# Performance work log

Measured on AMD Instinct MI355X. Metric: run time of the kernel, lower is better.

Reference implementation:

```python
import jax, jax.numpy as jnp
import numpy as np

B, N, D, H, L, M, V, F = 4, 2048, 1024, 16, 4, 256, 32000, 4096
DH = D // H  # 64
KEPS = 1e-4  # performer softmax-kernel eps


def layer_norm(x, g, b, eps=1e-5):
    mu = x.mean(-1, keepdims=True)
    var = ((x - mu) ** 2).mean(-1, keepdims=True)
    return (x - mu) * jax.lax.rsqrt(var + eps) * g + b


def softmax_kernel(data, proj, is_query):
    # data: [B,H,N,DH], proj: [M,DH] -> phi(data): [B,H,N,M]
    dn = data.shape[-1] ** -0.25  # d^{-1/4} normalizer
    ratio = proj.shape[0] ** -0.5
    dd = jnp.einsum('bhnd,md->bhnm', dn * data, proj)
    diag = (data * data).sum(-1, keepdims=True) * 0.5 * dn * dn
    if is_query:
        mx = jnp.max(dd, axis=-1, keepdims=True)
    else:
        mx = jnp.max(dd, axis=(-2, -1), keepdims=True)
    return ratio * (jnp.exp(dd - diag - mx) + KEPS)


def setup_inputs() -> dict:
    key = jax.random.key(0)
    ks = iter(jax.random.split(key, 16))
    p = lambda shape: jax.random.normal(next(ks), shape, jnp.float32) * 0.02
    return {
        'x': jax.random.randint(next(ks), (B, N), 0, V, jnp.int32),
        'mask': jnp.ones((B, N), jnp.bool_),
        'tok_emb': p((V, D)),
        'pos_emb': p((N, D)),
        'ln1_g': jnp.ones((L, D), jnp.float32), 'ln1_b': jnp.zeros((L, D), jnp.float32),
        'wq': p((L, D, D)), 'bq': jnp.zeros((L, D), jnp.float32),
        'wk': p((L, D, D)), 'bk': jnp.zeros((L, D), jnp.float32),
        'wv': p((L, D, D)), 'bv': jnp.zeros((L, D), jnp.float32),
        'wo': p((L, D, D)), 'bo': jnp.zeros((L, D), jnp.float32),
        'proj': jax.random.normal(next(ks), (L, M, DH), jnp.float32),
        'ln2_g': jnp.ones((L, D), jnp.float32), 'ln2_b': jnp.zeros((L, D), jnp.float32),
        'w1': p((L, D, F)), 'b1': jnp.zeros((L, F), jnp.float32),
        'w2': p((L, F, D)), 'b2': jnp.zeros((L, D), jnp.float32),
    }


def reference(x, mask, tok_emb, pos_emb, ln1_g, ln1_b, wq, bq, wk, bk, wv, bv,
              wo, bo, proj, ln2_g, ln2_b, w1, b1, w2, b2):
    h = tok_emb[x] + pos_emb[jnp.arange(N)]  # [B,N,D]
    mask4 = mask[:, None, :, None]  # [B,1,N,1]

    def split_heads(t):  # [B,N,D] -> [B,H,N,DH]
        return t.reshape(B, N, H, DH).transpose(0, 2, 1, 3)

    def layer(h, params):
        (g1, c1, Wq, Bq, Wk, Bk, Wv, Bv, Wo, Bo, P, g2, c2, W1, B1, W2, B2) = params
        z = layer_norm(h, g1, c1)
        q = split_heads(z @ Wq + Bq)
        k = split_heads(z @ Wk + Bk)
        v = split_heads(z @ Wv + Bv)
        v = jnp.where(mask4, v, 0.0)  # performer masks only v
        qp = softmax_kernel(q, P, True)   # [B,H,N,M]
        kp = softmax_kernel(k, P, False)  # [B,H,N,M]
        d_inv = 1.0 / jnp.einsum('bhnm,bhm->bhn', qp, kp.sum(-2))
        ctx = jnp.einsum('bhnm,bhnd->bhmd', kp, v)  # [B,H,M,DH]
        attn = jnp.einsum('bhmd,bhnm,bhn->bhnd', ctx, qp, d_inv)
        attn = attn.transpose(0, 2, 1, 3).reshape(B, N, D)
        h = h + attn @ Wo + Bo
        z = layer_norm(h, g2, c2)
        h = h + jax.nn.gelu(z @ W1 + B1, approximate=False) @ W2 + B2
        return h, None

    h, _ = jax.lax.scan(layer, h, (ln1_g, ln1_b, wq, bq, wk, bk, wv, bv,
                                   wo, bo, proj, ln2_g, ln2_b, w1, b1, w2, b2))
    return h.mean(1)  # [B,D]
```

## Files before the change

kernel.cpp:

```cpp
#include <hip/hip_runtime.h>
#include <hip/hip_bf16.h>

typedef unsigned short u16;
typedef unsigned int u32;
typedef __attribute__((ext_vector_type(8))) short short8v;
typedef __attribute__((ext_vector_type(4))) float f32x4;

#define BB    4
#define NN    2048
#define DDIM  1024
#define HH    16
#define DH    64
#define MM    256
#define FDIM  4096
#define LL    4
#define QLD   3072

static constexpr float DN_    = 0.35355339059327373f;
static constexpr float RATIO_ = 0.0625f;
static constexpr float KEPS_  = 1e-4f;

__device__ __forceinline__ short f2bs(float f) {
  __hip_bfloat16 h = __float2bfloat16(f);
  return *(short*)&h;
}
__device__ __forceinline__ float bs2f(short s) {
  return __uint_as_float(((unsigned)(u16)s) << 16);
}

__device__ __forceinline__ void gload_lds16(const void* g, void* l) {
  __builtin_amdgcn_global_load_lds(
      (const __attribute__((address_space(1))) u32*)g,
      (__attribute__((address_space(3))) u32*)l, 16, 0, 0);
}

__global__ __launch_bounds__(256) void k_sentinel(float* __restrict__ out, float val) {
  int i = blockIdx.x * 256 + threadIdx.x;
  if (i < BB * DDIM) out[i] = val;
}

__global__ __launch_bounds__(256) void k_embed(const int* __restrict__ x,
    const float* __restrict__ tok, const float* __restrict__ pos,
    float* __restrict__ h) {
  int r = blockIdx.x;
  int n = r & (NN - 1);
  int id = x[r];
  const float* tr = tok + (size_t)id * DDIM;
  const float* pr = pos + (size_t)n * DDIM;
  float* hr = h + (size_t)r * DDIM;
  for (int d = threadIdx.x; d < DDIM; d += 256)
    hr[d] = tr[d] + pr[d];
}

__global__ __launch_bounds__(256) void k_ln(const float* __restrict__ in,
    const float* __restrict__ g, const float* __restrict__ b,
    __hip_bfloat16* __restrict__ out) {
  int r = blockIdx.x, t = threadIdx.x;
  const float* xr = in + (size_t)r * DDIM;
  float v[4], s = 0.f, s2 = 0.f;
#pragma unroll
  for (int i = 0; i < 4; i++) {
    v[i] = xr[t + i * 256];
    s += v[i]; s2 += v[i] * v[i];
  }
#pragma unroll
  for (int o = 32; o > 0; o >>= 1) { s += __shfl_down(s, o); s2 += __shfl_down(s2, o); }
  __shared__ float ws[8];
  int wid = t >> 6, lane = t & 63;
  if (lane == 0) { ws[wid] = s; ws[4 + wid] = s2; }
  __syncthreads();
  s = ws[0] + ws[1] + ws[2] + ws[3];
  s2 = ws[4] + ws[5] + ws[6] + ws[7];
  float mu = s * (1.f / DDIM);
  float var = s2 * (1.f / DDIM) - mu * mu;
  float rstd = rsqrtf(var + 1e-5f);
  __hip_bfloat16* orow = out + (size_t)r * DDIM;
#pragma unroll
  for (int i = 0; i < 4; i++) {
    int d = t + i * 256;
    orow[d] = __float2bfloat16((v[i] - mu) * rstd * g[d] + b[d]);
  }
}

__global__ __launch_bounds__(256) void k_wt(const float* __restrict__ W,
    __hip_bfloat16* __restrict__ Wt, int K, int N) {
  __shared__ float tl[64][68];
  int t = threadIdx.x;
  int n0 = blockIdx.x * 64, k0 = blockIdx.y * 64;
#pragma unroll
  for (int i = 0; i < 4; i++) {
    int kl = (t >> 4) + i * 16;
    float4 f = *(const float4*)&W[(size_t)(k0 + kl) * N + n0 + (t & 15) * 4];
    tl[kl][(t & 15) * 4 + 0] = f.x;
    tl[kl][(t & 15) * 4 + 1] = f.y;
    tl[kl][(t & 15) * 4 + 2] = f.z;
    tl[kl][(t & 15) * 4 + 3] = f.w;
  }
  __syncthreads();
  int nl = t >> 2;
#pragma unroll
  for (int i = 0; i < 4; i++) {
    int kl = (t & 3) * 4 + i * 16;
    size_t ob = (size_t)(n0 + nl) * K + k0 + kl;
    Wt[ob + 0] = __float2bfloat16(tl[kl + 0][nl]);
    Wt[ob + 1] = __float2bfloat16(tl[kl + 1][nl]);
    Wt[ob + 2] = __float2bfloat16(tl[kl + 2][nl]);
    Wt[ob + 3] = __float2bfloat16(tl[kl + 3][nl]);
  }
}

__global__ __launch_bounds__(256) void k_catb(const float* __restrict__ bq,
    const float* __restrict__ bk, const float* __restrict__ bv,
    float* __restrict__ dst) {
  int i = blockIdx.x * 256 + threadIdx.x;
  dst[i] = i < 1024 ? bq[i] : (i < 2048 ? bk[i - 1024] : bv[i - 2048]);
}

template <bool GELU, bool RES, bool OUTF32>
__global__ __launch_bounds__(256) void k_gemm_mfma(
    const u16* __restrict__ A, const u16* __restrict__ Bt,
    const float* __restrict__ bias, const float* __restrict__ Cin,
    void* __restrict__ Cout, int M, int K, int Nc) {
  __shared__ short As[2][128 * 32];
  __shared__ short Bs[2][128 * 32];
  int t = threadIdx.x;
  int lane = t & 63, w = t >> 6;
  int wr = w >> 1, wc = w & 1;
  int nwg = gridDim.x * gridDim.y;
  int id = blockIdx.y * gridDim.x + blockIdx.x;
  int swz = (id & 7) * (nwg >> 3) + (id >> 3);
  int bx = swz % gridDim.x, by = swz / gridDim.x;
  int row0 = by * 128, col0 = bx * 128;
  f32x4 acc[4][4];
  f32x4 z4 = {0.f, 0.f, 0.f, 0.f};
#pragma unroll
  for (int i = 0; i < 4; i++)
#pragma unroll
    for (int j = 0; j < 4; j++) acc[i][j] = z4;
  int fr = lane & 15;
  int fc = lane >> 4;
  int c0 = t, c1 = 256 + t;
  int r0 = c0 >> 2, cl0 = (c0 & 3) ^ ((r0 >> 1) & 3);
  int r1 = c1 >> 2, cl1 = (c1 & 3) ^ ((r1 >> 1) & 3);
  const u16* Arow0 = A + (size_t)(row0 + r0) * K + cl0 * 8;
  const u16* Arow1 = A + (size_t)(row0 + r1) * K + cl1 * 8;
  const u16* Brow0 = Bt + (size_t)(col0 + r0) * K + cl0 * 8;
  const u16* Brow1 = Bt + (size_t)(col0 + r1) * K + cl1 * 8;

  auto STG = [&](int bi, int kk) {
    gload_lds16(Arow0 + kk, As[bi] + c0 * 8);
    gload_lds16(Arow1 + kk, As[bi] + c1 * 8);
    gload_lds16(Brow0 + kk, Bs[bi] + c0 * 8);
    gload_lds16(Brow1 + kk, Bs[bi] + c1 * 8);
  };
  auto COMPUTE = [&](int bi) {
    short8v af[4], bfr[4];
#pragma unroll
    for (int f = 0; f < 4; f++) {
      int ra = wr * 64 + f * 16 + fr;
      af[f] = *(const short8v*)(As[bi] + ra * 32 + (fc ^ ((ra >> 1) & 3)) * 8);
      int rb = wc * 64 + f * 16 + fr;
      bfr[f] = *(const short8v*)(Bs[bi] + rb * 32 + (fc ^ ((rb >> 1) & 3)) * 8);
    }
#pragma unroll
    for (int fi = 0; fi < 4; fi++)
#pragma unroll
      for (int fj = 0; fj < 4; fj++)
        acc[fi][fj] = __builtin_amdgcn_mfma_f32_16x16x32_bf16(
            af[fi], bfr[fj], acc[fi][fj], 0, 0, 0);
  };

  STG(0, 0);
  __syncthreads();
  int cur = 0;
  for (int k0 = 0; k0 + 32 < K; k0 += 32) {
    STG(cur ^ 1, k0 + 32);
    COMPUTE(cur);
    __syncthreads();
    cur ^= 1;
  }
  COMPUTE(cur);
#pragma unroll
  for (int fi = 0; fi < 4; fi++) {
#pragma unroll
    for (int fj = 0; fj < 4; fj++) {
#pragma unroll
      for (int ri = 0; ri < 4; ri++) {
        int row = row0 + wr * 64 + fi * 16 + (lane >> 4) * 4 + ri;
        int col = col0 + wc * 64 + fj * 16 + fr;
        float vv = acc[fi][fj][ri] + bias[col];
        if (GELU) vv = 0.5f * vv * (1.f + erff(vv * 0.70710678118f));
        if (RES) vv += Cin[(size_t)row * Nc + col];
        if (OUTF32) ((float*)Cout)[(size_t)row * Nc + col] = vv;
        else ((__hip_bfloat16*)Cout)[(size_t)row * Nc + col] = __float2bfloat16(vv);
      }
    }
  }
}

__global__ __launch_bounds__(256) void k_kv(const u16* __restrict__ kq,
    const u16* __restrict__ vq, const float* __restrict__ P,
    float* __restrict__ es, float* __restrict__ mxc, float* __restrict__ svc,
    float* __restrict__ ctx_part) {
  int bh = blockIdx.x >> 2, chunk = blockIdx.x & 3;
  int b = bh >> 4, hh = bh & 15;
  int t = threadIdx.x, lane = t & 63, w = t >> 6;
  int fr = lane & 15, kc = lane >> 4;
  __shared__ short Pl[256 * 64];
  __shared__ short ksl[32 * 64];
  __shared__ short vtl[64 * 32];
  __shared__ short kpl[256 * 32];
  __shared__ float dgs[32];
  __shared__ float wredk[4];
  __shared__ float svl[32][64];
#pragma unroll
  for (int i = 0; i < 8; i++) {
    int e = i * 256 + t;
    int m = e >> 3, j = e & 7;
    float4 f0 = *(const float4*)&P[m * 64 + j * 8];
    float4 f1 = *(const float4*)&P[m * 64 + j * 8 + 4];
    short* dst = Pl + m * 64 + ((j ^ (m & 7)) << 3);
    dst[0] = f2bs(f0.x); dst[1] = f2bs(f0.y); dst[2] = f2bs(f0.z); dst[3] = f2bs(f0.w);
    dst[4] = f2bs(f1.x); dst[5] = f2bs(f1.y); dst[6] = f2bs(f1.z); dst[7] = f2bs(f1.w);
  }
  f32x4 z4 = {0.f, 0.f, 0.f, 0.f};
  f32x4 accc[4][4];
#pragma unroll
  for (int i = 0; i < 4; i++)
#pragma unroll
    for (int j = 0; j < 4; j++) accc[i][j] = z4;
  float ksp[4] = {0.f, 0.f, 0.f, 0.f};
  float svp[8] = {0.f, 0.f, 0.f, 0.f, 0.f, 0.f, 0.f, 0.f};
  float m_run = -3e38f;
  int r8 = t >> 3, j8 = t & 7;
  for (int tile = 0; tile < 16; ++tile) {
    int n0 = chunk * 512 + tile * 32;
    __syncthreads();
    {
      size_t gk = ((size_t)(b * NN) + n0 + r8) * QLD + hh * 64 + j8 * 8;
      short8v k8 = *(const short8v*)(kq + gk);
      *(short8v*)(ksl + r8 * 64 + ((j8 ^ (r8 & 7)) << 3)) = k8;
      float s2 = 0.f;
#pragma unroll
      for (int ii = 0; ii < 8; ii++) { float rv = bs2f(k8[ii]); s2 += rv * rv; }
      s2 += __shfl_down(s2, 4); s2 += __shfl_down(s2, 2); s2 += __shfl_down(s2, 1);
      if (j8 == 0) dgs[r8] = 0.0625f * s2;
      short8v v8 = *(const short8v*)(vq + gk);
#pragma unroll
      for (int ii = 0; ii < 8; ii++) {
        int d = j8 * 8 + ii;
        vtl[d * 32 + (((r8 >> 3) ^ ((d >> 1) & 3)) << 3) + (r8 & 7)] = v8[ii];
        svp[ii] += bs2f(v8[ii]);
      }
    }
    __syncthreads();
    f32x4 accd[2][4];
#pragma unroll
    for (int nt = 0; nt < 2; nt++)
#pragma unroll
      for (int mt = 0; mt < 4; mt++) accd[nt][mt] = z4;
#pragma unroll
    for (int s = 0; s < 2; s++) {
      short8v afr[2];
#pragma unroll
      for (int nt = 0; nt < 2; nt++) {
        int rr = nt * 16 + fr;
        afr[nt] = *(const short8v*)(ksl + rr * 64 + (((s * 4 + kc) ^ (rr & 7)) << 3));
      }
#pragma unroll
      for (int mt = 0; mt < 4; mt++) {
        int m = w * 64 + mt * 16 + fr;
        short8v bfp = *(const short8v*)(Pl + m * 64 + (((s * 4 + kc) ^ (m & 7)) << 3));
#pragma unroll
        for (int nt = 0; nt < 2; nt++)
          accd[nt][mt] = __builtin_amdgcn_mfma_f32_16x16x32_bf16(afr[nt], bfp, accd[nt][mt], 0, 0, 0);
      }
    }
    float tm = -3e38f;
#pragma unroll
    for (int nt = 0; nt < 2; nt++)
#pragma unroll
      for (int mt = 0; mt < 4; mt++) {
        accd[nt][mt] = accd[nt][mt] * DN_;
        tm = fmaxf(tm, fmaxf(fmaxf(accd[nt][mt][0], accd[nt][mt][1]),
                             fmaxf(accd[nt][mt][2], accd[nt][mt][3])));
      }
#pragma unroll
    for (int o = 32; o > 0; o >>= 1) tm = fmaxf(tm, __shfl_xor(tm, o));
    if (lane == 0) wredk[w] = tm;
    __syncthreads();
    float bm = fmaxf(fmaxf(wredk[0], wredk[1]), fmaxf(wredk[2], wredk[3]));
    float nm = fmaxf(m_run, bm);
    float fac = expf(m_run - nm);
#pragma unroll
    for (int mt = 0; mt < 4; mt++) {
      ksp[mt] *= fac;
#pragma unroll
      for (int dt = 0; dt < 4; dt++) accc[mt][dt] = accc[mt][dt] * fac;
    }
    m_run = nm;
#pragma unroll
    for (int nt = 0; nt < 2; nt++)
#pragma unroll
      for (int mt = 0; mt < 4; mt++)
#pragma unroll
        for (int ri = 0; ri < 4; ri++) {
          int n = nt * 16 + kc * 4 + ri;
          int m = w * 64 + mt * 16 + fr;
          float kpv = expf(accd[nt][mt][ri] - dgs[n] - m_run);
          ksp[mt] += kpv;
          kpl[m * 32 + (((n >> 3) ^ ((m >> 1) & 3)) << 3) + (n & 7)] = f2bs(kpv);
        }
    short8v bvv[4];
#pragma unroll
    for (int dt = 0; dt < 4; dt++) {
      int d = dt * 16 + fr;
      bvv[dt] = *(const short8v*)(vtl + d * 32 + ((kc ^ ((d >> 1) & 3)) << 3));
    }
#pragma unroll
    for (int mt = 0; mt < 4; mt++) {
      int m = w * 64 + mt * 16 + fr;
      short8v ak = *(const short8v*)(kpl + m * 32 + ((kc ^ ((m >> 1) & 3)) << 3));
#pragma unroll
      for (int dt = 0; dt < 4; dt++)
        accc[mt][dt] = __builtin_amdgcn_mfma_f32_16x16x32_bf16(ak, bvv[dt], accc[mt][dt], 0, 0, 0);
    }
  }
#pragma unroll
  for (int mt = 0; mt < 4; mt++) {
    float vv = ksp[mt];
    vv += __shfl_xor(vv, 16);
    vv += __shfl_xor(vv, 32);
    if (lane < 16)
      es[((size_t)bh * 4 + chunk) * MM + w * 64 + mt * 16 + lane] = vv;
  }
  if (t == 0) mxc[bh * 4 + chunk] = m_run;
#pragma unroll
  for (int ii = 0; ii < 8; ii++) svl[r8][j8 * 8 + ii] = svp[ii];
  __syncthreads();
  if (t < 64) {
    float s = 0.f;
#pragma unroll
    for (int r = 0; r < 32; r++) s += svl[r][t];
    svc[((size_t)bh * 4 + chunk) * 64 + t] = s;
  }
  size_t base = ((size_t)(chunk * 64 + bh)) * MM * DH;
#pragma unroll
  for (int mt = 0; mt < 4; mt++)
#pragma unroll
    for (int dt = 0; dt < 4; dt++)
#pragma unroll
      for (int ri = 0; ri < 4; ri++) {
        int m = w * 64 + mt * 16 + kc * 4 + ri;
        int d = dt * 16 + fr;
        ctx_part[base + m * 64 + d] = accc[mt][dt][ri];
      }
}

__global__ __launch_bounds__(256) void k_ctxred(const float* __restrict__ part,
    const float* __restrict__ es, const float* __restrict__ mxc,
    const float* __restrict__ svc, float* __restrict__ ksum,
    u16* __restrict__ ctxT) {
  int bh = blockIdx.x, t = threadIdx.x;
  __shared__ float tl[64][65];
  __shared__ float facs[4];
  __shared__ float svg[64];
  float mg = fmaxf(fmaxf(mxc[bh * 4 + 0], mxc[bh * 4 + 1]),
                   fmaxf(mxc[bh * 4 + 2], mxc[bh * 4 + 3]));
  if (t < 4) facs[t] = expf(mxc[bh * 4 + t] - mg);
  if (t >= 64 && t < 128) {
    int d = t - 64;
    svg[d] = svc[((size_t)bh * 4 + 0) * 64 + d] + svc[((size_t)bh * 4 + 1) * 64 + d] +
             svc[((size_t)bh * 4 + 2) * 64 + d] + svc[((size_t)bh * 4 + 3) * 64 + d];
  }
  __syncthreads();
  float f0 = facs[0], f1 = facs[1], f2 = facs[2], f3 = facs[3];
  {
    size_t eb = (size_t)bh * 4 * MM;
    float s = es[eb + t] * f0 + es[eb + MM + t] * f1 +
              es[eb + 2 * MM + t] * f2 + es[eb + 3 * MM + t] * f3;
    ksum[bh * MM + t] = RATIO_ * (s + KEPS_ * 2048.0f);
  }
  const size_t CH = (size_t)64 * MM * DH;
  for (int mt = 0; mt < 4; mt++) {
    __syncthreads();
#pragma unroll
    for (int i = 0; i < 16; i++) {
      int e = i * 256 + t;
      int ml = e >> 6, d = e & 63;
      size_t off = (size_t)bh * MM * DH + (size_t)(mt * 64 + ml) * 64 + d;
      float ev = part[off] * f0 + part[CH + off] * f1 +
                 part[2 * CH + off] * f2 + part[3 * CH + off] * f3;
      tl[ml][d] = RATIO_ * (ev + KEPS_ * svg[d]);
    }
    __syncthreads();
#pragma unroll
    for (int i = 0; i < 16; i++) {
      int e = i * 256 + t;
      int d = e >> 6, ml = e & 63;
      ctxT[((size_t)bh * 64 + d) * 256 + mt * 64 + ml] = (u16)f2bs(tl[ml][d]);
    }
  }
}

__global__ __launch_bounds__(256) void k_attn_fused(const u16* __restrict__ q,
    const float* __restrict__ P, const float* __restrict__ ksum,
    const u16* __restrict__ ctxT, __hip_bfloat16* __restrict__ attn) {
  int bh = blockIdx.x >> 5, rb = blockIdx.x & 31;
  int b = bh >> 4, hh = bh & 15;
  int n0 = rb * 64;
  int t = threadIdx.x, lane = t & 63, w = t >> 6;
  int fr = lane & 15, kc = lane >> 4;
  __shared__ short qsl[64 * 64];
  __shared__ short qpl[64 * 256];
  __shared__ short ctl[64 * 256];
  __shared__ float dgs[64];
  __shared__ float ks_l[MM];
  __shared__ float wred[4][64];
  __shared__ float mx_l[64];
  __shared__ float inv_l[64];
  short8v pf[4][2];
#pragma unroll
  for (int mt = 0; mt < 4; mt++)
#pragma unroll
    for (int s = 0; s < 2; s++) {
      int m = w * 64 + mt * 16 + fr;
      const float* src = P + m * 64 + s * 32 + kc * 8;
      float4 f0 = *(const float4*)src;
      float4 f1 = *(const float4*)(src + 4);
      short8v pv;
      pv[0] = f2bs(f0.x); pv[1] = f2bs(f0.y); pv[2] = f2bs(f0.z); pv[3] = f2bs(f0.w);
      pv[4] = f2bs(f1.x); pv[5] = f2bs(f1.y); pv[6] = f2bs(f1.z); pv[7] = f2bs(f1.w);
      pf[mt][s] = pv;
    }
  ks_l[t] = ksum[bh * MM + t];
  {
    int rr = t >> 2, j4 = t & 3;
    size_t gq = ((size_t)(b * NN) + n0 + rr) * QLD + hh * 64 + j4 * 16;
    short8v q0 = *(const short8v*)(q + gq);
    short8v q1 = *(const short8v*)(q + gq + 8);
    *(short8v*)(qsl + rr * 64 + (((2 * j4) ^ (rr & 7)) << 3)) = q0;
    *(short8v*)(qsl + rr * 64 + (((2 * j4 + 1) ^ (rr & 7)) << 3)) = q1;
    float s2 = 0.f;
#pragma unroll
    for (int ii = 0; ii < 8; ii++) {
      float a = bs2f(q0[ii]), c = bs2f(q1[ii]);
      s2 += a * a + c * c;
    }
    s2 += __shfl_down(s2, 2); s2 += __shfl_down(s2, 1);
    if (j4 == 0) dgs[rr] = 0.0625f * s2;
  }
#pragma unroll
  for (int i = 0; i < 8; i++) {
    int e = i * 256 + t;
    int d = e >> 5, c = e & 31;
    short8v cv = *(const short8v*)(ctxT + ((size_t)bh * 64 + d) * 256 + c * 8);
    *(short8v*)(ctl + d * 256 + ((c ^ (d & 7)) << 3)) = cv;
  }
  __syncthreads();
  f32x4 z4 = {0.f, 0.f, 0.f, 0.f};
  f32x4 accd[4][4];
#pragma unroll
  for (int i = 0; i < 4; i++)
#pragma unroll
    for (int j = 0; j < 4; j++) accd[i][j] = z4;
#pragma unroll
  for (int s = 0; s < 2; s++) {
    short8v afr[4];
#pragma unroll
    for (int nt = 0; nt < 4; nt++) {
      int rr = nt * 16 + fr;
      afr[nt] = *(const short8v*)(qsl + rr * 64 + (((s * 4 + kc) ^ (rr & 7)) << 3));
    }
#pragma unroll
    for (int mt = 0; mt < 4; mt++)
#pragma unroll
      for (int nt = 0; nt < 4; nt++)
        accd[nt][mt] = __builtin_amdgcn_mfma_f32_16x16x32_bf16(afr[nt], pf[mt][s], accd[nt][mt], 0, 0, 0);
  }
#pragma unroll
  for (int i = 0; i < 4; i++)
#pragma unroll
    for (int j = 0; j < 4; j++) accd[i][j] = accd[i][j] * DN_;
  {
    float pmx[16];
#pragma unroll
    for (int nt = 0; nt < 4; nt++)
#pragma unroll
      for (int ri = 0; ri < 4; ri++) {
        float m_ = fmaxf(fmaxf(accd[nt][0][ri], accd[nt][1][ri]),
                         fmaxf(accd[nt][2][ri], accd[nt][3][ri]));
#pragma unroll
        for (int o = 1; o < 16; o <<= 1) m_ = fmaxf(m_, __shfl_xor(m_, o));
        pmx[nt * 4 + ri] = m_;
      }
    if (fr == 0) {
#pragma unroll
      for (int nt = 0; nt < 4; nt++)
#pragma unroll
        for (int ri = 0; ri < 4; ri++)
          wred[w][nt * 16 + kc * 4 + ri] = pmx[nt * 4 + ri];
    }
  }
  __syncthreads();
  if (t < 64)
    mx_l[t] = fmaxf(fmaxf(wred[0][t], wred[1][t]), fmaxf(wred[2][t], wred[3][t]));
  __syncthreads();
  {
    float sp[16];
#pragma unroll
    for (int i = 0; i < 16; i++) sp[i] = 0.f;
#pragma unroll
    for (int nt = 0; nt < 4; nt++)
#pragma unroll
      for (int mt = 0; mt < 4; mt++)
#pragma unroll
        for (int ri = 0; ri < 4; ri++) {
          int n = nt * 16 + kc * 4 + ri;
          int m = w * 64 + mt * 16 + fr;
          float kpv = RATIO_ * (expf(accd[nt][mt][ri] - dgs[n] - mx_l[n]) + KEPS_);
          sp[nt * 4 + ri] += kpv * ks_l[m];
          int c = m >> 3;
          qpl[n * 256 + ((c ^ (n & 7)) << 3) + (m & 7)] = f2bs(kpv);
        }
#pragma unroll
    for (int i = 0; i < 16; i++) {
#pragma unroll
      for (int o = 1; o < 16; o <<= 1) sp[i] += __shfl_xor(sp[i], o);
    }
    if (fr == 0) {
#pragma unroll
      for (int nt = 0; nt < 4; nt++)
#pragma unroll
        for (int ri = 0; ri < 4; ri++)
          wred[w][nt * 16 + kc * 4 + ri] = sp[nt * 4 + ri];
    }
  }
  __syncthreads();
  if (t < 64)
    inv_l[t] = 1.f / (wred[0][t] + wred[1][t] + wred[2][t] + wred[3][t]);
  __syncthreads();
  f32x4 acc2[4];
#pragma unroll
  for (int dt = 0; dt < 4; dt++) acc2[dt] = z4;
  int nrow = w * 16 + fr;
#pragma unroll
  for (int ks = 0; ks < 8; ks++) {
    int c = ks * 4 + kc;
    short8v aq = *(const short8v*)(qpl + nrow * 256 + ((c ^ (nrow & 7)) << 3));
#pragma unroll
    for (int dt = 0; dt < 4; dt++) {
      int d = dt * 16 + fr;
      short8v bc = *(const short8v*)(ctl + d * 256 + ((c ^ (d & 7)) << 3));
      acc2[dt] = __builtin_amdgcn_mfma_f32_16x16x32_bf16(aq, bc, acc2[dt], 0, 0, 0);
    }
  }
#pragma unroll
  for (int dt = 0; dt < 4; dt++)
#pragma unroll
    for (int ri = 0; ri < 4; ri++) {
      int n = w * 16 + kc * 4 + ri;
      int d = dt * 16 + fr;
      attn[((size_t)(b * NN) + n0 + n) * DDIM + hh * 64 + d] =
          __float2bfloat16(acc2[dt][ri] * inv_l[n]);
    }
}

__global__ __launch_bounds__(256) void k_mean1(const float* __restrict__ h,
                                               float* __restrict__ part) {
  int c = blockIdx.x >> 2, b = blockIdx.x & 3;
  int t = threadIdx.x;
  float s0 = 0.f, s1 = 0.f, s2 = 0.f, s3 = 0.f;
  for (int n = c * 32; n < c * 32 + 32; n++) {
    float4 f = *(const float4*)&h[((size_t)b * NN + n) * DDIM + t * 4];
    s0 += f.x; s1 += f.y; s2 += f.z; s3 += f.w;
  }
  float* p = part + (size_t)c * (BB * DDIM) + b * DDIM + t * 4;
  p[0] = s0; p[1] = s1; p[2] = s2; p[3] = s3;
}
__global__ __launch_bounds__(256) void k_mean2(const float* __restrict__ part,
                                               float* __restrict__ out) {
  int idx = blockIdx.x * 256 + threadIdx.x;
  float s = 0.f;
  for (int c = 0; c < 64; c++) s += part[(size_t)c * (BB * DDIM) + idx];
  out[idx] = s * (1.f / NN);
}

extern "C" void kernel_launch(void* const* d_in, const int* in_sizes, int n_in,
                              void* d_out, int out_size, void* d_ws, size_t ws_size,
                              hipStream_t stream) {
  static const long long EXP[21] = {
      8192, 8192, 32768000, 2097152, 4096, 4096,
      4194304, 4096, 4194304, 4096, 4194304, 4096, 4194304, 4096,
      65536, 4096, 4096, 16777216, 16384, 16777216, 4096
  };
  const size_t NEED_WS = 197559552;
  float sentinel = 0.f;
  if (n_in != 21) {
    sentinel = 100000.f + 100.f * (float)n_in;
  } else {
    for (int i = 0; i < 21; i++)
      if ((long long)in_sizes[i] != EXP[i]) { sentinel = 1000.f + 100.f * i; break; }
  }
  if (sentinel == 0.f && out_size != BB * DDIM) sentinel = 6000.f;
  if (sentinel == 0.f && ws_size < NEED_WS) {
    float units = (float)(ws_size / (32ull << 20));
    if (units > 40.f) units = 40.f;
    sentinel = 5000.f + 100.f * units;
  }
  if (sentinel != 0.f) {
    k_sentinel<<<16, 256, 0, stream>>>((float*)d_out, sentinel);
    return;
  }

  const int* x = (const int*)d_in[0];
  const float* tok  = (const float*)d_in[2];
  const float* pos  = (const float*)d_in[3];
  const float* ln1g = (const float*)d_in[4];
  const float* ln1b = (const float*)d_in[5];
  const float* wq   = (const float*)d_in[6];
  const float* bq   = (const float*)d_in[7];
  const float* wk   = (const float*)d_in[8];
  const float* bk   = (const float*)d_in[9];
  const float* wv   = (const float*)d_in[10];
  const float* bv   = (const float*)d_in[11];
  const float* wo   = (const float*)d_in[12];
  const float* bo   = (const float*)d_in[13];
  const float* proj = (const float*)d_in[14];
  const float* ln2g = (const float*)d_in[15];
  const float* ln2b = (const float*)d_in[16];
  const float* w1   = (const float*)d_in[17];
  const float* b1   = (const float*)d_in[18];
  const float* w2   = (const float*)d_in[19];
  const float* b2   = (const float*)d_in[20];

  const int BN = BB * NN;
  const size_t SZ = (size_t)BN * DDIM;
  const size_t MEG = 1048576;
  float* ws    = (float*)d_ws;
  float* h     = ws;
  u16* qkvb    = (u16*)(ws + SZ);
  __hip_bfloat16* zb   = (__hip_bfloat16*)(ws + 4 * SZ);
  float* ctx   = ws + 4 * SZ + SZ / 2;
  float* ksum  = ctx + (size_t)BB * HH * MM * DH;
  float* bmaxp = ksum + BB * HH * MM;
  float* bcat  = bmaxp + 4096;
  float* mxp   = bmaxp + BB * HH * 128;
  __hip_bfloat16* wt = (__hip_bfloat16*)(mxp + 64);
  float* ctxp  = (float*)(wt + 12 * MEG);
  float* esb   = ctxp + 4 * MEG;
  float* mxcb  = esb + 65536;
  float* svcb  = mxcb + 256;
  u16* ctxT    = (u16*)ctx;
  __hip_bfloat16* ff1b = (__hip_bfloat16*)qkvb;
  __hip_bfloat16* zab  = (__hip_bfloat16*)ctxp;
  float* meanp = ctxp;

  k_embed<<<BN, 256, 0, stream>>>(x, tok, pos, h);

  for (int l = 0; l < LL; l++) {
    const float* Wq = wq + (size_t)l * DDIM * DDIM;
    const float* Wk = wk + (size_t)l * DDIM * DDIM;
    const float* Wv = wv + (size_t)l * DDIM * DDIM;
    const float* Wo = wo + (size_t)l * DDIM * DDIM;
    const float* W1 = w1 + (size_t)l * DDIM * FDIM;
    const float* W2 = w2 + (size_t)l * FDIM * DDIM;
    const float* Pl = proj + (size_t)l * MM * DH;
    __hip_bfloat16* wtq = wt;
    __hip_bfloat16* wtk = wt + 1 * MEG;
    __hip_bfloat16* wtv = wt + 2 * MEG;
    __hip_bfloat16* wto = wt + 3 * MEG;
    __hip_bfloat16* wt1 = wt + 4 * MEG;
    __hip_bfloat16* wt2 = wt + 8 * MEG;

    k_wt<<<dim3(16, 16), 256, 0, stream>>>(Wq, wtq, DDIM, DDIM);
    k_wt<<<dim3(16, 16), 256, 0, stream>>>(Wk, wtk, DDIM, DDIM);
    k_wt<<<dim3(16, 16), 256, 0, stream>>>(Wv, wtv, DDIM, DDIM);
    k_wt<<<dim3(16, 16), 256, 0, stream>>>(Wo, wto, DDIM, DDIM);
    k_wt<<<dim3(64, 16), 256, 0, stream>>>(W1, wt1, DDIM, FDIM);
    k_wt<<<dim3(16, 64), 256, 0, stream>>>(W2, wt2, FDIM, DDIM);
    k_catb<<<12, 256, 0, stream>>>(bq + l * DDIM, bk + l * DDIM, bv + l * DDIM, bcat);

    k_ln<<<BN, 256, 0, stream>>>(h, ln1g + l * DDIM, ln1b + l * DDIM, zb);

    dim3 gQKV(QLD / 128, BN / 128);
    k_gemm_mfma<false, false, false><<<gQKV, 256, 0, stream>>>(
        (const u16*)zb, (const u16*)wtq, bcat, nullptr, qkvb, BN, DDIM, QLD);

    k_kv<<<BB * HH * 4, 256, 0, stream>>>(qkvb + 1024, qkvb + 2048, Pl,
                                          esb, mxcb, svcb, ctxp);
    k_ctxred<<<BB * HH, 256, 0, stream>>>(ctxp, esb, mxcb, svcb, ksum, ctxT);
    k_attn_fused<<<BB * HH * 32, 256, 0, stream>>>(qkvb, Pl, ksum, ctxT, zab);

    dim3 gO(DDIM / 128, BN / 128);
    k_gemm_mfma<false, true, true><<<gO, 256, 0, stream>>>(
        (const u16*)zab, (const u16*)wto, bo + l * DDIM, h, h, BN, DDIM, DDIM);

    k_ln<<<BN, 256, 0, stream>>>(h, ln2g + l * DDIM, ln2b + l * DDIM, zb);
    dim3 g1(FDIM / 128, BN / 128);
    k_gemm_mfma<true, false, false><<<g1, 256, 0, stream>>>(
        (const u16*)zb, (const u16*)wt1, b1 + l * FDIM, nullptr, ff1b, BN, DDIM, FDIM);
    dim3 g2(DDIM / 128, BN / 128);
    k_gemm_mfma<false, true, true><<<g2, 256, 0, stream>>>(
        (const u16*)ff1b, (const u16*)wt2, b2 + l * DDIM, h, h, BN, FDIM, DDIM);
  }

  k_mean1<<<256, 256, 0, stream>>>(h, meanp);
  k_mean2<<<16, 256, 0, stream>>>(meanp, (float*)d_out);
}
```

Before: 2.079 ms.

## Fuse embed with LN, batch weight transposes, split k_kv over feature halves

Several unrelated changes land together. Embedding is fused with the first LayerNorm. The six per-layer weight-transpose launches and the bias concat are merged into one kernel. k_kv is split across two halves of the random-feature dimension, doubling its grid, and each half keeps its own running max, which k_ctxred reconciles. erff in the GELU epilogue is replaced by a polynomial erf approximation, and expf by __expf. The goals are fewer launches, better CU occupancy for the key/value reduction and cheaper transcendentals, at the cost of small numerical deviations.

```diff
diff --git a/kernel.cpp b/kernel.cpp
--- a/kernel.cpp
+++ b/kernel.cpp
@@ -27,6 +27,14 @@
 __device__ __forceinline__ float bs2f(short s) {
   return __uint_as_float(((unsigned)(u16)s) << 16);
 }
+__device__ __forceinline__ float erf_fast(float x) {
+  float ax = fabsf(x);
+  float t = 1.f / (1.f + 0.3275911f * ax);
+  float y = t * (0.254829592f + t * (-0.284496736f + t * (1.421413741f +
+            t * (-1.453152027f + t * 1.061405429f))));
+  float r = 1.f - y * __expf(-ax * ax);
+  return copysignf(r, x);
+}
 
 __device__ __forceinline__ void gload_lds16(const void* g, void* l) {
   __builtin_amdgcn_global_load_lds(
@@ -39,17 +47,41 @@
   if (i < BB * DDIM) out[i] = val;
 }
 
-__global__ __launch_bounds__(256) void k_embed(const int* __restrict__ x,
+__global__ __launch_bounds__(256) void k_embed_ln(const int* __restrict__ x,
     const float* __restrict__ tok, const float* __restrict__ pos,
-    float* __restrict__ h) {
-  int r = blockIdx.x;
+    const float* __restrict__ g, const float* __restrict__ b,
+    float* __restrict__ h, __hip_bfloat16* __restrict__ zb) {
+  int r = blockIdx.x, t = threadIdx.x;
   int n = r & (NN - 1);
   int id = x[r];
   const float* tr = tok + (size_t)id * DDIM;
   const float* pr = pos + (size_t)n * DDIM;
   float* hr = h + (size_t)r * DDIM;
-  for (int d = threadIdx.x; d < DDIM; d += 256)
-    hr[d] = tr[d] + pr[d];
+  float v[4], s = 0.f, s2 = 0.f;
+#pragma unroll
+  for (int i = 0; i < 4; i++) {
+    int d = t + i * 256;
+    v[i] = tr[d] + pr[d];
+    hr[d] = v[i];
+    s += v[i]; s2 += v[i] * v[i];
+  }
+#pragma unroll
+  for (int o = 32; o > 0; o >>= 1) { s += __shfl_down(s, o); s2 += __shfl_down(s2, o); }
+  __shared__ float ws[8];
+  int wid = t >> 6, lane = t & 63;
+  if (lane == 0) { ws[wid] = s; ws[4 + wid] = s2; }
+  __syncthreads();
+  s = ws[0] + ws[1] + ws[2] + ws[3];
+  s2 = ws[4] + ws[5] + ws[6] + ws[7];
+  float mu = s * (1.f / DDIM);
+  float var = s2 * (1.f / DDIM) - mu * mu;
+  float rstd = rsqrtf(var + 1e-5f);
+  __hip_bfloat16* orow = zb + (size_t)r * DDIM;
+#pragma unroll
+  for (int i = 0; i < 4; i++) {
+    int d = t + i * 256;
+    orow[d] = __float2bfloat16((v[i] - mu) * rstd * g[d] + b[d]);
+  }
 }
 
 __global__ __launch_bounds__(256) void k_ln(const float* __restrict__ in,
@@ -82,11 +114,40 @@
   }
 }
 
-__global__ __launch_bounds__(256) void k_wt(const float* __restrict__ W,
-    __hip_bfloat16* __restrict__ Wt, int K, int N) {
+__global__ __launch_bounds__(256) void k_wtall(const float* __restrict__ Wq,
+    const float* __restrict__ Wk, const float* __restrict__ Wv,
+    const float* __restrict__ Wo, const float* __restrict__ W1,
+    const float* __restrict__ W2, const float* __restrict__ bq,
+    const float* __restrict__ bk, const float* __restrict__ bv,
+    __hip_bfloat16* __restrict__ wt, float* __restrict__ bcat) {
+  int id = blockIdx.x;
+  int t = threadIdx.x;
+  if (id >= 3072) {
+    int i = (id - 3072) * 256 + t;
+    bcat[i] = i < 1024 ? bq[i] : (i < 2048 ? bk[i - 1024] : bv[i - 2048]);
+    return;
+  }
+  const float* W;
+  __hip_bfloat16* Wt;
+  int K, N, n0, k0;
+  if (id < 1024) {
+    int which = id >> 8, local = id & 255;
+    W = which == 0 ? Wq : which == 1 ? Wk : which == 2 ? Wv : Wo;
+    Wt = wt + (size_t)which * 1048576;
+    K = 1024; N = 1024;
+    n0 = (local & 15) * 64; k0 = (local >> 4) * 64;
+  } else if (id < 2048) {
+    int local = id - 1024;
+    W = W1; Wt = wt + (size_t)4 * 1048576;
+    K = 1024; N = 4096;
+    n0 = (local & 63) * 64; k0 = (local >> 6) * 64;
+  } else {
+    int local = id - 2048;
+    W = W2; Wt = wt + (size_t)8 * 1048576;
+    K = 4096; N = 1024;
+    n0 = (local & 15) * 64; k0 = (local >> 4) * 64;
+  }
   __shared__ float tl[64][68];
-  int t = threadIdx.x;
-  int n0 = blockIdx.x * 64, k0 = blockIdx.y * 64;
 #pragma unroll
   for (int i = 0; i < 4; i++) {
     int kl = (t >> 4) + i * 16;
@@ -107,13 +168,6 @@
     Wt[ob + 2] = __float2bfloat16(tl[kl + 2][nl]);
     Wt[ob + 3] = __float2bfloat16(tl[kl + 3][nl]);
   }
-}
-
-__global__ __launch_bounds__(256) void k_catb(const float* __restrict__ bq,
-    const float* __restrict__ bk, const float* __restrict__ bv,
-    float* __restrict__ dst) {
-  int i = blockIdx.x * 256 + threadIdx.x;
-  dst[i] = i < 1024 ? bq[i] : (i < 2048 ? bk[i - 1024] : bv[i - 2048]);
 }
 
 template <bool GELU, bool RES, bool OUTF32>
@@ -189,7 +243,7 @@
         int row = row0 + wr * 64 + fi * 16 + (lane >> 4) * 4 + ri;
         int col = col0 + wc * 64 + fj * 16 + fr;
         float vv = acc[fi][fj][ri] + bias[col];
-        if (GELU) vv = 0.5f * vv * (1.f + erff(vv * 0.70710678118f));
+        if (GELU) vv = 0.5f * vv * (1.f + erf_fast(vv * 0.70710678118f));
         if (RES) vv += Cin[(size_t)row * Nc + col];
         if (OUTF32) ((float*)Cout)[(size_t)row * Nc + col] = vv;
         else ((__hip_bfloat16*)Cout)[(size_t)row * Nc + col] = __float2bfloat16(vv);
@@ -202,34 +256,37 @@
     const u16* __restrict__ vq, const float* __restrict__ P,
     float* __restrict__ es, float* __restrict__ mxc, float* __restrict__ svc,
     float* __restrict__ ctx_part) {
-  int bh = blockIdx.x >> 2, chunk = blockIdx.x & 3;
+  int bh = blockIdx.x >> 3;
+  int chunk = (blockIdx.x >> 1) & 3;
+  int mh = blockIdx.x & 1;
   int b = bh >> 4, hh = bh & 15;
   int t = threadIdx.x, lane = t & 63, w = t >> 6;
   int fr = lane & 15, kc = lane >> 4;
-  __shared__ short Pl[256 * 64];
+  __shared__ short Pl[128 * 64];
   __shared__ short ksl[32 * 64];
   __shared__ short vtl[64 * 32];
-  __shared__ short kpl[256 * 32];
+  __shared__ short kpl[128 * 32];
   __shared__ float dgs[32];
   __shared__ float wredk[4];
   __shared__ float svl[32][64];
 #pragma unroll
-  for (int i = 0; i < 8; i++) {
+  for (int i = 0; i < 4; i++) {
     int e = i * 256 + t;
     int m = e >> 3, j = e & 7;
-    float4 f0 = *(const float4*)&P[m * 64 + j * 8];
-    float4 f1 = *(const float4*)&P[m * 64 + j * 8 + 4];
+    const float* src = P + (size_t)(mh * 128 + m) * 64 + j * 8;
+    float4 f0 = *(const float4*)src;
+    float4 f1 = *(const float4*)(src + 4);
     short* dst = Pl + m * 64 + ((j ^ (m & 7)) << 3);
     dst[0] = f2bs(f0.x); dst[1] = f2bs(f0.y); dst[2] = f2bs(f0.z); dst[3] = f2bs(f0.w);
     dst[4] = f2bs(f1.x); dst[5] = f2bs(f1.y); dst[6] = f2bs(f1.z); dst[7] = f2bs(f1.w);
   }
   f32x4 z4 = {0.f, 0.f, 0.f, 0.f};
-  f32x4 accc[4][4];
-#pragma unroll
-  for (int i = 0; i < 4; i++)
+  f32x4 accc[2][4];
+#pragma unroll
+  for (int i = 0; i < 2; i++)
 #pragma unroll
     for (int j = 0; j < 4; j++) accc[i][j] = z4;
-  float ksp[4] = {0.f, 0.f, 0.f, 0.f};
+  float ksp[2] = {0.f, 0.f};
   float svp[8] = {0.f, 0.f, 0.f, 0.f, 0.f, 0.f, 0.f, 0.f};
   float m_run = -3e38f;
   int r8 = t >> 3, j8 = t & 7;
@@ -254,11 +311,11 @@
       }
     }
     __syncthreads();
-    f32x4 accd[2][4];
+    f32x4 accd[2][2];
 #pragma unroll
     for (int nt = 0; nt < 2; nt++)
 #pragma unroll
-      for (int mt = 0; mt < 4; mt++) accd[nt][mt] = z4;
+      for (int mt = 0; mt < 2; mt++) accd[nt][mt] = z4;
 #pragma unroll
     for (int s = 0; s < 2; s++) {
       short8v afr[2];
@@ -268,9 +325,9 @@
         afr[nt] = *(const short8v*)(ksl + rr * 64 + (((s * 4 + kc) ^ (rr & 7)) << 3));
       }
 #pragma unroll
-      for (int mt = 0; mt < 4; mt++) {
-        int m = w * 64 + mt * 16 + fr;
-        short8v bfp = *(const short8v*)(Pl + m * 64 + (((s * 4 + kc) ^ (m & 7)) << 3));
+      for (int mt = 0; mt < 2; mt++) {
+        int ml = w * 32 + mt * 16 + fr;
+        short8v bfp = *(const short8v*)(Pl + ml * 64 + (((s * 4 + kc) ^ (ml & 7)) << 3));
 #pragma unroll
         for (int nt = 0; nt < 2; nt++)
           accd[nt][mt] = __builtin_amdgcn_mfma_f32_16x16x32_bf16(afr[nt], bfp, accd[nt][mt], 0, 0, 0);
@@ -280,7 +337,7 @@
 #pragma unroll
     for (int nt = 0; nt < 2; nt++)
 #pragma unroll
-      for (int mt = 0; mt < 4; mt++) {
+      for (int mt = 0; mt < 2; mt++) {
         accd[nt][mt] = accd[nt][mt] * DN_;
         tm = fmaxf(tm, fmaxf(fmaxf(accd[nt][mt][0], accd[nt][mt][1]),
                              fmaxf(accd[nt][mt][2], accd[nt][mt][3])));
@@ -291,9 +348,9 @@
     __syncthreads();
     float bm = fmaxf(fmaxf(wredk[0], wredk[1]), fmaxf(wredk[2], wredk[3]));
     float nm = fmaxf(m_run, bm);
-    float fac = expf(m_run - nm);
-#pragma unroll
-    for (int mt = 0; mt < 4; mt++) {
+    float fac = __expf(m_run - nm);
+#pragma unroll
+    for (int mt = 0; mt < 2; mt++) {
       ksp[mt] *= fac;
 #pragma unroll
       for (int dt = 0; dt < 4; dt++) accc[mt][dt] = accc[mt][dt] * fac;
@@ -302,14 +359,14 @@
 #pragma unroll
     for (int nt = 0; nt < 2; nt++)
 #pragma unroll
-      for (int mt = 0; mt < 4; mt++)
+      for (int mt = 0; mt < 2; mt++)
 #pragma unroll
         for (int ri = 0; ri < 4; ri++) {
           int n = nt * 16 + kc * 4 + ri;
-          int m = w * 64 + mt * 16 + fr;
-          float kpv = expf(accd[nt][mt][ri] - dgs[n] - m_run);
+          int ml = w * 32 + mt * 16 + fr;
+          float kpv = __expf(accd[nt][mt][ri] - dgs[n] - m_run);
           ksp[mt] += kpv;
-          kpl[m * 32 + (((n >> 3) ^ ((m >> 1) & 3)) << 3) + (n & 7)] = f2bs(kpv);
+          kpl[ml * 32 + (((n >> 3) ^ ((ml >> 1) & 3)) << 3) + (n & 7)] = f2bs(kpv);
         }
     short8v bvv[4];
 #pragma unroll
@@ -318,27 +375,27 @@
       bvv[dt] = *(const short8v*)(vtl + d * 32 + ((kc ^ ((d >> 1) & 3)) << 3));
     }
 #pragma unroll
-    for (int mt = 0; mt < 4; mt++) {
-      int m = w * 64 + mt * 16 + fr;
-      short8v ak = *(const short8v*)(kpl + m * 32 + ((kc ^ ((m >> 1) & 3)) << 3));
+    for (int mt = 0; mt < 2; mt++) {
+      int ml = w * 32 + mt * 16 + fr;
+      short8v ak = *(const short8v*)(kpl + ml * 32 + ((kc ^ ((ml >> 1) & 3)) << 3));
 #pragma unroll
       for (int dt = 0; dt < 4; dt++)
         accc[mt][dt] = __builtin_amdgcn_mfma_f32_16x16x32_bf16(ak, bvv[dt], accc[mt][dt], 0, 0, 0);
     }
   }
 #pragma unroll
-  for (int mt = 0; mt < 4; mt++) {
+  for (int mt = 0; mt < 2; mt++) {
     float vv = ksp[mt];
     vv += __shfl_xor(vv, 16);
     vv += __shfl_xor(vv, 32);
     if (lane < 16)
-      es[((size_t)bh * 4 + chunk) * MM + w * 64 + mt * 16 + lane] = vv;
-  }
-  if (t == 0) mxc[bh * 4 + chunk] = m_run;
+      es[((size_t)bh * 4 + chunk) * MM + mh * 128 + w * 32 + mt * 16 + lane] = vv;
+  }
+  if (t == 0) mxc[((size_t)bh * 4 + chunk) * 2 + mh] = m_run;
 #pragma unroll
   for (int ii = 0; ii < 8; ii++) svl[r8][j8 * 8 + ii] = svp[ii];
   __syncthreads();
-  if (t < 64) {
+  if (mh == 0 && t < 64) {
     float s = 0.f;
 #pragma unroll
     for (int r = 0; r < 32; r++) s += svl[r][t];
@@ -346,14 +403,14 @@
   }
   size_t base = ((size_t)(chunk * 64 + bh)) * MM * DH;
 #pragma unroll
-  for (int mt = 0; mt < 4; mt++)
+  for (int mt = 0; mt < 2; mt++)
 #pragma unroll
     for (int dt = 0; dt < 4; dt++)
 #pragma unroll
       for (int ri = 0; ri < 4; ri++) {
-        int m = w * 64 + mt * 16 + kc * 4 + ri;
+        int mg = mh * 128 + w * 32 + mt * 16 + kc * 4 + ri;
         int d = dt * 16 + fr;
-        ctx_part[base + m * 64 + d] = accc[mt][dt][ri];
+        ctx_part[base + mg * 64 + d] = accc[mt][dt][ri];
       }
 }
 
@@ -363,26 +420,30 @@
     u16* __restrict__ ctxT) {
   int bh = blockIdx.x, t = threadIdx.x;
   __shared__ float tl[64][65];
-  __shared__ float facs[4];
+  __shared__ float facs[8];
   __shared__ float svg[64];
-  float mg = fmaxf(fmaxf(mxc[bh * 4 + 0], mxc[bh * 4 + 1]),
-                   fmaxf(mxc[bh * 4 + 2], mxc[bh * 4 + 3]));
-  if (t < 4) facs[t] = expf(mxc[bh * 4 + t] - mg);
+  float mg = -3e38f;
+#pragma unroll
+  for (int i = 0; i < 8; i++) mg = fmaxf(mg, mxc[(size_t)bh * 8 + i]);
+  if (t < 8) facs[t] = __expf(mxc[(size_t)bh * 8 + t] - mg);
   if (t >= 64 && t < 128) {
     int d = t - 64;
     svg[d] = svc[((size_t)bh * 4 + 0) * 64 + d] + svc[((size_t)bh * 4 + 1) * 64 + d] +
              svc[((size_t)bh * 4 + 2) * 64 + d] + svc[((size_t)bh * 4 + 3) * 64 + d];
   }
   __syncthreads();
-  float f0 = facs[0], f1 = facs[1], f2 = facs[2], f3 = facs[3];
   {
     size_t eb = (size_t)bh * 4 * MM;
-    float s = es[eb + t] * f0 + es[eb + MM + t] * f1 +
-              es[eb + 2 * MM + t] * f2 + es[eb + 3 * MM + t] * f3;
+    int mhb = t >> 7;
+    float s = es[eb + t] * facs[0 * 2 + mhb] + es[eb + MM + t] * facs[1 * 2 + mhb] +
+              es[eb + 2 * MM + t] * facs[2 * 2 + mhb] + es[eb + 3 * MM + t] * facs[3 * 2 + mhb];
     ksum[bh * MM + t] = RATIO_ * (s + KEPS_ * 2048.0f);
   }
   const size_t CH = (size_t)64 * MM * DH;
   for (int mt = 0; mt < 4; mt++) {
+    int mhb = mt >> 1;
+    float f0 = facs[0 * 2 + mhb], f1 = facs[1 * 2 + mhb];
+    float f2 = facs[2 * 2 + mhb], f3 = facs[3 * 2 + mhb];
     __syncthreads();
 #pragma unroll
     for (int i = 0; i < 16; i++) {
@@ -518,7 +579,7 @@
         for (int ri = 0; ri < 4; ri++) {
           int n = nt * 16 + kc * 4 + ri;
           int m = w * 64 + mt * 16 + fr;
-          float kpv = RATIO_ * (expf(accd[nt][mt][ri] - dgs[n] - mx_l[n]) + KEPS_);
+          float kpv = RATIO_ * (__expf(accd[nt][mt][ri] - dgs[n] - mx_l[n]) + KEPS_);
           sp[nt * 4 + ri] += kpv * ks_l[m];
           int c = m >> 3;
           qpl[n * 256 + ((c ^ (n & 7)) << 3) + (m & 7)] = f2bs(kpv);
@@ -650,13 +711,13 @@
   float* ctxp  = (float*)(wt + 12 * MEG);
   float* esb   = ctxp + 4 * MEG;
   float* mxcb  = esb + 65536;
-  float* svcb  = mxcb + 256;
+  float* svcb  = mxcb + 512;
   u16* ctxT    = (u16*)ctx;
   __hip_bfloat16* ff1b = (__hip_bfloat16*)qkvb;
   __hip_bfloat16* zab  = (__hip_bfloat16*)ctxp;
   float* meanp = ctxp;
 
-  k_embed<<<BN, 256, 0, stream>>>(x, tok, pos, h);
+  k_embed_ln<<<BN, 256, 0, stream>>>(x, tok, pos, ln1g, ln1b, h, zb);
 
   for (int l = 0; l < LL; l++) {
     const float* Wq = wq + (size_t)l * DDIM * DDIM;
@@ -667,27 +728,22 @@
     const float* W2 = w2 + (size_t)l * FDIM * DDIM;
     const float* Pl = proj + (size_t)l * MM * DH;
     __hip_bfloat16* wtq = wt;
-    __hip_bfloat16* wtk = wt + 1 * MEG;
-    __hip_bfloat16* wtv = wt + 2 * MEG;
     __hip_bfloat16* wto = wt + 3 * MEG;
     __hip_bfloat16* wt1 = wt + 4 * MEG;
     __hip_bfloat16* wt2 = wt + 8 * MEG;
 
-    k_wt<<<dim3(16, 16), 256, 0, stream>>>(Wq, wtq, DDIM, DDIM);
-    k_wt<<<dim3(16, 16), 256, 0, stream>>>(Wk, wtk, DDIM, DDIM);
-    k_wt<<<dim3(16, 16), 256, 0, stream>>>(Wv, wtv, DDIM, DDIM);
-    k_wt<<<dim3(16, 16), 256, 0, stream>>>(Wo, wto, DDIM, DDIM);
-    k_wt<<<dim3(64, 16), 256, 0, stream>>>(W1, wt1, DDIM, FDIM);
-    k_wt<<<dim3(16, 64), 256, 0, stream>>>(W2, wt2, FDIM, DDIM);
-    k_catb<<<12, 256, 0, stream>>>(bq + l * DDIM, bk + l * DDIM, bv + l * DDIM, bcat);
-
-    k_ln<<<BN, 256, 0, stream>>>(h, ln1g + l * DDIM, ln1b + l * DDIM, zb);
+    k_wtall<<<3084, 256, 0, stream>>>(Wq, Wk, Wv, Wo, W1, W2,
+                                      bq + l * DDIM, bk + l * DDIM, bv + l * DDIM,
+                                      wt, bcat);
+
+    if (l > 0)
+      k_ln<<<BN, 256, 0, stream>>>(h, ln1g + l * DDIM, ln1b + l * DDIM, zb);
 
     dim3 gQKV(QLD / 128, BN / 128);
     k_gemm_mfma<false, false, false><<<gQKV, 256, 0, stream>>>(
         (const u16*)zb, (const u16*)wtq, bcat, nullptr, qkvb, BN, DDIM, QLD);
 
-    k_kv<<<BB * HH * 4, 256, 0, stream>>>(qkvb + 1024, qkvb + 2048, Pl,
+    k_kv<<<BB * HH * 8, 256, 0, stream>>>(qkvb + 1024, qkvb + 2048, Pl,
                                           esb, mxcb, svcb, ctxp);
     k_ctxred<<<BB * HH, 256, 0, stream>>>(ctxp, esb, mxcb, svcb, ksum, ctxT);
     k_attn_fused<<<BB * HH * 32, 256, 0, stream>>>(qkvb, Pl, ksum, ctxT, zab);
```

Measured after the change: 1.952 ms. -6.1%, faster.
